# Performance work log

Hardware: AMD Instinct MI355X
Metric: run time of the kernel (lower is better)

The kernel has to match this reference:

```python
import jax, jax.numpy as jnp
import numpy as np

B, F, A, H = 131072, 32, 8, 64  # batch, n_features, n_actions, hidden

def setup_inputs() -> dict:
    key = jax.random.key(0)
    k = jax.random.split(key, 6)
    return {
        "f_t": jax.random.normal(k[0], (B, F), dtype=jnp.float32),
        "a_t": jax.random.normal(k[1], (B, A), dtype=jnp.float32),
        "W1": jax.random.normal(k[2], (F, F + A, H), dtype=jnp.float32) * 0.1,
        "b1": jax.random.normal(k[3], (F, H), dtype=jnp.float32) * 0.1,
        "W2": jax.random.normal(k[4], (F, H), dtype=jnp.float32) * 0.1,
        "b2": jax.random.normal(k[5], (F,), dtype=jnp.float32) * 0.1,
    }

def reference(f_t, a_t, W1, b1, W2, b2):
    # fa_t: [B, F+A] shared input to all F submodels
    fa_t = jnp.concatenate((f_t, a_t), axis=1)
    # Batched grouped-GEMM over the F independent submodels.
    h = jax.nn.relu(jnp.einsum('bi,fih->bfh', fa_t, W1) + b1)  # [B, F, H]
    f_t1 = jnp.einsum('bfh,fh->bf', h, W2) + b2                 # [B, F]
    # skip_connection=True
    return f_t1 + f_t
```

## Files before the change

kernel.cpp:

```cpp
#include <hip/hip_runtime.h>

#define B_TOTAL 131072
#define NF 32
#define NA 8
#define NH 64

using frag_ab = __attribute__((ext_vector_type(8))) short;
using f32x16  = __attribute__((ext_vector_type(16))) float;
typedef int   v2i __attribute__((ext_vector_type(2)));
typedef float v2f __attribute__((ext_vector_type(2)));

__device__ __forceinline__ unsigned short f2bf(float x) {
  unsigned u = __float_as_uint(x);
  u = (u + 0x7FFFu + ((u >> 16) & 1u)) >> 16;
  return (unsigned short)u;
}

__global__ void pack_w1_kernel(const float* __restrict__ W1, const float* __restrict__ b1,
                               unsigned short* __restrict__ w1p) {
  int idx = blockIdx.x * 256 + threadIdx.x;
  int j = idx & 7, l = (idx >> 3) & 63, tq = idx >> 9;
  int q = tq % 6, f = tq / 6;
  int ht = q / 3, kt = q % 3;
  int h = ht * 32 + (l & 31);
  int i = kt * 16 + ((l >> 5) << 3) + j;
  float v = 0.0f;
  if (i < NF + NA)       v = W1[(f * (NF + NA) + i) * NH + h];
  else if (i == NF + NA) v = b1[f * NH + h];
  w1p[idx] = f2bf(v);
}

__global__ void pack_w2_kernel(const float* __restrict__ W2, float* __restrict__ w2p) {
  int idx = blockIdx.x * 256 + threadIdx.x;
  int r = idx & 15, ht = (idx >> 4) & 1, g = (idx >> 5) & 1, f = idx >> 6;
  w2p[idx] = W2[f * NH + ht * 32 + (r & 3) + 8 * (r >> 2) + 4 * g];
}

__device__ __forceinline__ v2f pk_fma(v2f a, v2f b, v2f c) {
  v2f d;
  asm("v_pk_fma_f32 %0, %1, %2, %3" : "=v"(d) : "v"(a), "v"(b), "v"(c));
  return d;
}

__device__ __forceinline__ float xor32_add(float v) {
  v2i p = __builtin_amdgcn_permlane32_swap(__float_as_int(v), __float_as_int(v), false, false);
  return __int_as_float(p.x) + __int_as_float(p.y);
}

__global__ __launch_bounds__(256, 4) void fused_mlp_kernel(
    const float* __restrict__ ft, const float* __restrict__ at,
    const unsigned short* __restrict__ w1p, const float* __restrict__ w2p,
    const float* __restrict__ b2, float* __restrict__ out) {
  __shared__ __align__(16) unsigned short wlds[2][6144];

  const int t = threadIdx.x;
  const int wv = t >> 6;
  const int l = t & 63;
  const int g = l >> 5;
  const int lc = l & 31;
  const long rowb = (long)blockIdx.x * 128 + wv * 32;

  {
    const unsigned short* src = w1p + t * 8;
#pragma unroll
    for (int k = 0; k < 3; ++k)
      __builtin_amdgcn_global_load_lds((const __attribute__((address_space(1))) void*)(src + k * 2048),
                                       (__attribute__((address_space(3))) void*)(&wlds[0][k * 2048 + t * 8]), 16, 0, 0);
  }

  frag_ab bfr[3];
  {
    const long b = rowb + lc;
    const float* fr = ft + b * NF;
    float tmp[8];
#pragma unroll
    for (int kt = 0; kt < 2; ++kt) {
      *(float4*)tmp       = *(const float4*)(fr + kt * 16 + g * 8);
      *(float4*)(tmp + 4) = *(const float4*)(fr + kt * 16 + g * 8 + 4);
      frag_ab fb;
#pragma unroll
      for (int j = 0; j < 8; ++j) fb[j] = (short)f2bf(tmp[j]);
      bfr[kt] = fb;
    }
    *(float4*)tmp       = *(const float4*)(at + b * NA);
    *(float4*)(tmp + 4) = *(const float4*)(at + b * NA + 4);
    frag_ab fb;
#pragma unroll
    for (int j = 0; j < 8; ++j) {
      unsigned short bias = (j == 0) ? (unsigned short)0x3F80 : (unsigned short)0;
      fb[j] = (short)((g == 0) ? f2bf(tmp[j]) : bias);
    }
    bfr[2] = fb;
  }

  const f32x16 zero16 = {0.f,0.f,0.f,0.f,0.f,0.f,0.f,0.f,0.f,0.f,0.f,0.f,0.f,0.f,0.f,0.f};
  float res[NF];

  for (int r = 0; r < 16; ++r) {
    __syncthreads();

    if (r < 15) {
      const unsigned short* src = w1p + (r + 1) * 6144 + t * 8;
#pragma unroll
      for (int k = 0; k < 3; ++k)
        __builtin_amdgcn_global_load_lds((const __attribute__((address_space(1))) void*)(src + k * 2048),
                                         (__attribute__((address_space(3))) void*)(&wlds[(r + 1) & 1][k * 2048 + t * 8]), 16, 0, 0);
    }

    const unsigned short* buf = wlds[r & 1];

#pragma unroll
    for (int fo = 0; fo < 2; ++fo) {
      const int f = r * 2 + fo;

      frag_ab wf[2][3];
#pragma unroll
      for (int ht = 0; ht < 2; ++ht)
#pragma unroll
        for (int kt = 0; kt < 3; ++kt)
          wf[ht][kt] = *(const frag_ab*)&buf[((fo * 6 + ht * 3 + kt) * 64 + l) * 8];

      float4 wq[8];
      const float4* wp = (const float4*)w2p + (f * 2 + g) * 8;
#pragma unroll
      for (int q = 0; q < 8; ++q) wq[q] = wp[q];

      f32x16 a0 = zero16, a1 = zero16;
#pragma unroll
      for (int kt = 0; kt < 3; ++kt) {
        a0 = __builtin_amdgcn_mfma_f32_32x32x16_bf16(wf[0][kt], bfr[kt], a0, 0, 0, 0);
        a1 = __builtin_amdgcn_mfma_f32_32x32x16_bf16(wf[1][kt], bfr[kt], a1, 0, 0, 0);
      }
      v2f ps0 = {0.f, 0.f}, ps1 = {0.f, 0.f};
#pragma unroll
      for (int rq = 0; rq < 4; ++rq) {
        float4 w0 = wq[rq], w1 = wq[4 + rq];
        v2f m;
        m[0] = fmaxf(a0[rq * 4 + 0], 0.f); m[1] = fmaxf(a0[rq * 4 + 1], 0.f);
        ps0 = pk_fma(m, (v2f){w0.x, w0.y}, ps0);
        m[0] = fmaxf(a0[rq * 4 + 2], 0.f); m[1] = fmaxf(a0[rq * 4 + 3], 0.f);
        ps0 = pk_fma(m, (v2f){w0.z, w0.w}, ps0);
        m[0] = fmaxf(a1[rq * 4 + 0], 0.f); m[1] = fmaxf(a1[rq * 4 + 1], 0.f);
        ps1 = pk_fma(m, (v2f){w1.x, w1.y}, ps1);
        m[0] = fmaxf(a1[rq * 4 + 2], 0.f); m[1] = fmaxf(a1[rq * 4 + 3], 0.f);
        ps1 = pk_fma(m, (v2f){w1.z, w1.w}, ps1);
      }
      float s = (ps0[0] + ps0[1]) + (ps1[0] + ps1[1]);
      res[f] = xor32_add(s);
    }
  }

  const long row = rowb + lc;
  const float* fr = ft + row * NF + g * 16;
  const float* bb = b2 + g * 16;
  float* op = out + row * NF + g * 16;
#pragma unroll
  for (int q = 0; q < 4; ++q) {
    float4 x = *(const float4*)(fr + q * 4);
    float4 bv = *(const float4*)(bb + q * 4);
    float4 o;
    o.x = res[g * 16 + q * 4 + 0] + bv.x + x.x;
    o.y = res[g * 16 + q * 4 + 1] + bv.y + x.y;
    o.z = res[g * 16 + q * 4 + 2] + bv.z + x.z;
    o.w = res[g * 16 + q * 4 + 3] + bv.w + x.w;
    *(float4*)(op + q * 4) = o;
  }
}

extern "C" void kernel_launch(void* const* d_in, const int* in_sizes, int n_in,
                              void* d_out, int out_size, void* d_ws, size_t ws_size,
                              hipStream_t stream) {
  const float* ft = (const float*)d_in[0];
  const float* at = (const float*)d_in[1];
  const float* W1 = (const float*)d_in[2];
  const float* b1 = (const float*)d_in[3];
  const float* W2 = (const float*)d_in[4];
  const float* b2 = (const float*)d_in[5];
  float* out = (float*)d_out;

  unsigned short* w1p = (unsigned short*)d_ws;
  float* w2p = (float*)((char*)d_ws + (1u << 18));

  pack_w1_kernel<<<384, 256, 0, stream>>>(W1, b1, w1p);
  pack_w2_kernel<<<16, 256, 0, stream>>>(W2, w2p);
  fused_mlp_kernel<<<B_TOTAL / 128, 256, 0, stream>>>(ft, at, w1p, w2p, b2, out);
}
```

Before: 64.73 us.

## Split feature groups across blocks with register-resident weights and separate add pass

Restructures the MLP kernel so each block owns a pair of submodels and keeps their W1/W2 fragments in registers, looping over 1024 batch rows. This removes the LDS double-buffering and per-round __syncthreads. Each block re-reads and re-converts f_t/a_t rows, so the input is read 16 times instead of once. Partial results go to a workspace, and a second kernel adds b2 and the skip connection, which costs extra global traffic and a launch.

```diff
diff --git a/kernel.cpp b/kernel.cpp
--- a/kernel.cpp
+++ b/kernel.cpp
@@ -47,94 +47,78 @@
   return __int_as_float(p.x) + __int_as_float(p.y);
 }
 
-__global__ __launch_bounds__(256, 4) void fused_mlp_kernel(
+__global__ __launch_bounds__(256, 2) void fused_mlp_kernel(
     const float* __restrict__ ft, const float* __restrict__ at,
     const unsigned short* __restrict__ w1p, const float* __restrict__ w2p,
-    const float* __restrict__ b2, float* __restrict__ out) {
-  __shared__ __align__(16) unsigned short wlds[2][6144];
-
+    float* __restrict__ ws) {
   const int t = threadIdx.x;
   const int wv = t >> 6;
   const int l = t & 63;
   const int g = l >> 5;
   const int lc = l & 31;
-  const long rowb = (long)blockIdx.x * 128 + wv * 32;
+  const int gf = blockIdx.x >> 7;
+  const int nb = blockIdx.x & 127;
 
-  {
-    const unsigned short* src = w1p + t * 8;
+  frag_ab wf[2][2][3];
 #pragma unroll
-    for (int k = 0; k < 3; ++k)
-      __builtin_amdgcn_global_load_lds((const __attribute__((address_space(1))) void*)(src + k * 2048),
-                                       (__attribute__((address_space(3))) void*)(&wlds[0][k * 2048 + t * 8]), 16, 0, 0);
-  }
+  for (int f2 = 0; f2 < 2; ++f2)
+#pragma unroll
+    for (int ht = 0; ht < 2; ++ht)
+#pragma unroll
+      for (int kt = 0; kt < 3; ++kt)
+        wf[f2][ht][kt] = *(const frag_ab*)(w1p + ((((gf * 2 + f2) * 6 + ht * 3 + kt) * 64 + l) * 8));
 
-  frag_ab bfr[3];
-  {
-    const long b = rowb + lc;
-    const float* fr = ft + b * NF;
-    float tmp[8];
+  float4 wq[2][8];
 #pragma unroll
-    for (int kt = 0; kt < 2; ++kt) {
-      *(float4*)tmp       = *(const float4*)(fr + kt * 16 + g * 8);
-      *(float4*)(tmp + 4) = *(const float4*)(fr + kt * 16 + g * 8 + 4);
-      frag_ab fb;
+  for (int f2 = 0; f2 < 2; ++f2) {
+    const float4* wp = (const float4*)w2p + (((gf * 2 + f2) * 2 + g)) * 8;
 #pragma unroll
-      for (int j = 0; j < 8; ++j) fb[j] = (short)f2bf(tmp[j]);
-      bfr[kt] = fb;
-    }
-    *(float4*)tmp       = *(const float4*)(at + b * NA);
-    *(float4*)(tmp + 4) = *(const float4*)(at + b * NA + 4);
-    frag_ab fb;
-#pragma unroll
-    for (int j = 0; j < 8; ++j) {
-      unsigned short bias = (j == 0) ? (unsigned short)0x3F80 : (unsigned short)0;
-      fb[j] = (short)((g == 0) ? f2bf(tmp[j]) : bias);
-    }
-    bfr[2] = fb;
+    for (int q = 0; q < 8; ++q) wq[f2][q] = wp[q];
   }
 
   const f32x16 zero16 = {0.f,0.f,0.f,0.f,0.f,0.f,0.f,0.f,0.f,0.f,0.f,0.f,0.f,0.f,0.f,0.f};
-  float res[NF];
 
-  for (int r = 0; r < 16; ++r) {
-    __syncthreads();
+  for (int it = 0; it < 8; ++it) {
+    const long rowb = (long)nb * 1024 + wv * 256 + it * 32;
 
-    if (r < 15) {
-      const unsigned short* src = w1p + (r + 1) * 6144 + t * 8;
+    frag_ab bfr[3];
+    {
+      const long b = rowb + lc;
+      const float* fr = ft + b * NF;
+      float tmp[8];
 #pragma unroll
-      for (int k = 0; k < 3; ++k)
-        __builtin_amdgcn_global_load_lds((const __attribute__((address_space(1))) void*)(src + k * 2048),
-                                         (__attribute__((address_space(3))) void*)(&wlds[(r + 1) & 1][k * 2048 + t * 8]), 16, 0, 0);
+      for (int kt = 0; kt < 2; ++kt) {
+        *(float4*)tmp       = *(const float4*)(fr + kt * 16 + g * 8);
+        *(float4*)(tmp + 4) = *(const float4*)(fr + kt * 16 + g * 8 + 4);
+        frag_ab fb;
+#pragma unroll
+        for (int j = 0; j < 8; ++j) fb[j] = (short)f2bf(tmp[j]);
+        bfr[kt] = fb;
+      }
+      *(float4*)tmp       = *(const float4*)(at + b * NA);
+      *(float4*)(tmp + 4) = *(const float4*)(at + b * NA + 4);
+      frag_ab fb;
+#pragma unroll
+      for (int j = 0; j < 8; ++j) {
+        unsigned short bias = (j == 0) ? (unsigned short)0x3F80 : (unsigned short)0;
+        fb[j] = (short)((g == 0) ? f2bf(tmp[j]) : bias);
+      }
+      bfr[2] = fb;
     }
 
-    const unsigned short* buf = wlds[r & 1];
-
+    float resv[2];
 #pragma unroll
-    for (int fo = 0; fo < 2; ++fo) {
-      const int f = r * 2 + fo;
-
-      frag_ab wf[2][3];
-#pragma unroll
-      for (int ht = 0; ht < 2; ++ht)
-#pragma unroll
-        for (int kt = 0; kt < 3; ++kt)
-          wf[ht][kt] = *(const frag_ab*)&buf[((fo * 6 + ht * 3 + kt) * 64 + l) * 8];
-
-      float4 wq[8];
-      const float4* wp = (const float4*)w2p + (f * 2 + g) * 8;
-#pragma unroll
-      for (int q = 0; q < 8; ++q) wq[q] = wp[q];
-
+    for (int f2 = 0; f2 < 2; ++f2) {
       f32x16 a0 = zero16, a1 = zero16;
 #pragma unroll
       for (int kt = 0; kt < 3; ++kt) {
-        a0 = __builtin_amdgcn_mfma_f32_32x32x16_bf16(wf[0][kt], bfr[kt], a0, 0, 0, 0);
-        a1 = __builtin_amdgcn_mfma_f32_32x32x16_bf16(wf[1][kt], bfr[kt], a1, 0, 0, 0);
+        a0 = __builtin_amdgcn_mfma_f32_32x32x16_bf16(wf[f2][0][kt], bfr[kt], a0, 0, 0, 0);
+        a1 = __builtin_amdgcn_mfma_f32_32x32x16_bf16(wf[f2][1][kt], bfr[kt], a1, 0, 0, 0);
       }
       v2f ps0 = {0.f, 0.f}, ps1 = {0.f, 0.f};
 #pragma unroll
       for (int rq = 0; rq < 4; ++rq) {
-        float4 w0 = wq[rq], w1 = wq[4 + rq];
+        float4 w0 = wq[f2][rq], w1 = wq[f2][4 + rq];
         v2f m;
         m[0] = fmaxf(a0[rq * 4 + 0], 0.f); m[1] = fmaxf(a0[rq * 4 + 1], 0.f);
         ps0 = pk_fma(m, (v2f){w0.x, w0.y}, ps0);
@@ -146,25 +130,32 @@
         ps1 = pk_fma(m, (v2f){w1.z, w1.w}, ps1);
       }
       float s = (ps0[0] + ps0[1]) + (ps1[0] + ps1[1]);
-      res[f] = xor32_add(s);
+      resv[f2] = xor32_add(s);
+    }
+
+    if (g == 0) {
+      float2 o; o.x = resv[0]; o.y = resv[1];
+      *(float2*)(ws + ((long)gf * B_TOTAL + rowb + lc) * 2) = o;
     }
   }
+}
 
-  const long row = rowb + lc;
-  const float* fr = ft + row * NF + g * 16;
-  const float* bb = b2 + g * 16;
-  float* op = out + row * NF + g * 16;
-#pragma unroll
-  for (int q = 0; q < 4; ++q) {
-    float4 x = *(const float4*)(fr + q * 4);
-    float4 bv = *(const float4*)(bb + q * 4);
-    float4 o;
-    o.x = res[g * 16 + q * 4 + 0] + bv.x + x.x;
-    o.y = res[g * 16 + q * 4 + 1] + bv.y + x.y;
-    o.z = res[g * 16 + q * 4 + 2] + bv.z + x.z;
-    o.w = res[g * 16 + q * 4 + 3] + bv.w + x.w;
-    *(float4*)(op + q * 4) = o;
-  }
+__global__ void add_kernel(const float* __restrict__ ws, const float* __restrict__ ft,
+                           const float* __restrict__ b2, float* __restrict__ out) {
+  int flat = blockIdx.x * 256 + threadIdx.x;
+  int f4 = flat & 7;
+  long b = flat >> 3;
+  const float2* s0 = (const float2*)ws + (long)(2 * f4) * B_TOTAL + b;
+  const float2* s1 = (const float2*)ws + (long)(2 * f4 + 1) * B_TOTAL + b;
+  float2 v0 = *s0, v1 = *s1;
+  float4 x  = *(const float4*)(ft + b * NF + f4 * 4);
+  float4 bb = *(const float4*)(b2 + f4 * 4);
+  float4 o;
+  o.x = v0.x + bb.x + x.x;
+  o.y = v0.y + bb.y + x.y;
+  o.z = v1.x + bb.z + x.z;
+  o.w = v1.y + bb.w + x.w;
+  *(float4*)(out + b * NF + f4 * 4) = o;
 }
 
 extern "C" void kernel_launch(void* const* d_in, const int* in_sizes, int n_in,
@@ -180,8 +171,10 @@
 
   unsigned short* w1p = (unsigned short*)d_ws;
   float* w2p = (float*)((char*)d_ws + (1u << 18));
+  float* ws  = (float*)((char*)d_ws + (1u << 20));
 
   pack_w1_kernel<<<384, 256, 0, stream>>>(W1, b1, w1p);
   pack_w2_kernel<<<16, 256, 0, stream>>>(W2, w2p);
-  fused_mlp_kernel<<<B_TOTAL / 128, 256, 0, stream>>>(ft, at, w1p, w2p, b2, out);
+  fused_mlp_kernel<<<2048, 256, 0, stream>>>(ft, at, w1p, w2p, ws);
+  add_kernel<<<B_TOTAL * 8 / 256, 256, 0, stream>>>(ws, ft, b2, out);
 }
```

New measurement: 78.18 us. 20.8% more time.
